# Kernel optimization log

Measured on AMD Instinct MI355X. Metric: run time of the kernel, lower is better.

The kernel has to match this reference:

```python
import jax, jax.numpy as jnp
import numpy as np

B, T, C = 16, 4096, 2048
H = 16
HS = C // H  # 128
SCALE = 1.0 / float(np.sqrt(HS))


def setup_inputs() -> dict:
    key = jax.random.key(0)
    k1, k2, k3, k4, k5 = jax.random.split(key, 5)
    x = jax.random.normal(k1, (B, 1, C), dtype=jnp.float32)
    k = jax.random.normal(k2, (B, H, T, HS), dtype=jnp.float32)
    v = jax.random.normal(k3, (B, H, T, HS), dtype=jnp.float32)
    # nn.Linear(dim, dim, bias=False) weights, applied as x @ W.T
    Wq = jax.random.normal(k4, (C, C), dtype=jnp.float32) * (1.0 / np.sqrt(C))
    Wp = jax.random.normal(k5, (C, C), dtype=jnp.float32) * (1.0 / np.sqrt(C))
    return {"x": x, "k": k, "v": v, "Wq": Wq, "Wp": Wp}


def reference(x, k, v, Wq, Wp):
    # decode branch: only last token of x is used
    q = x[:, -1, :] @ Wq.T                      # [B, C]
    q = q.reshape(B, H, HS)                     # [B, H, HS] (single query token)
    # att = (q * k).sum(-1) * scale  -> scores over cache length T
    att = jnp.einsum('bhd,bhtd->bht', q, k) * SCALE   # [B, H, T]
    att = jax.nn.softmax(att, axis=-1)
    # y = att @ v  -> [B, H, 1, HS], collapsed here
    y = jnp.einsum('bht,bhtd->bhd', att, v)     # [B, H, HS]
    y = y.reshape(B, 1, C)                      # transpose(1,2).view(B,1,C) equivalent for 1 token
    out = y @ Wp.T                              # [B, 1, C]; dropout is identity in eval
    return out
```

## Files before the change

### kernel.cpp

```cpp
#include <hip/hip_runtime.h>
#include <cmath>

#define C_DIM 2048
#define B_DIM 16
#define H_DIM 16
#define HS_DIM 128
#define T_DIM 4096
#define ATT_SCALE 0.08838834764831845f

__global__ __launch_bounds__(256) void gemv16_kernel(
    const float* __restrict__ X, const float* __restrict__ W,
    float* __restrict__ O) {
  const int lane = threadIdx.x & 63;
  const int wave = threadIdx.x >> 6;
  const int n = blockIdx.x * 4 + wave;
  const float* wrow = W + (size_t)n * C_DIM;

  float acc[B_DIM];
#pragma unroll
  for (int m = 0; m < B_DIM; ++m) acc[m] = 0.f;

#pragma unroll
  for (int i = 0; i < C_DIM / 256; ++i) {
    const int j = i * 256 + lane * 4;
    const float4 w4 = *reinterpret_cast<const float4*>(wrow + j);
#pragma unroll
    for (int m = 0; m < B_DIM; ++m) {
      const float4 x4 = *reinterpret_cast<const float4*>(X + m * C_DIM + j);
      acc[m] += w4.x * x4.x + w4.y * x4.y + w4.z * x4.z + w4.w * x4.w;
    }
  }

#pragma unroll
  for (int m = 0; m < B_DIM; ++m) {
#pragma unroll
    for (int mask = 32; mask >= 1; mask >>= 1)
      acc[m] += __shfl_xor(acc[m], mask, 64);
  }
  if (lane == 0) {
#pragma unroll
    for (int m = 0; m < B_DIM; ++m) O[(size_t)m * C_DIM + n] = acc[m];
  }
}

__global__ __launch_bounds__(1024) void attn_decode_kernel(
    const float* __restrict__ q, const float* __restrict__ k,
    const float* __restrict__ v, float* __restrict__ y) {
  const int bh = blockIdx.x;
  const int lane = threadIdx.x & 63;
  const int wave = threadIdx.x >> 6;
  const int half = lane >> 5;
  const int dl = lane & 31;

  const float4* kp = reinterpret_cast<const float4*>(k + (size_t)bh * T_DIM * HS_DIM);
  const float4* vp = reinterpret_cast<const float4*>(v + (size_t)bh * T_DIM * HS_DIM);
  const float4 qv = reinterpret_cast<const float4*>(q + (size_t)bh * HS_DIM)[dl];

  float m = -INFINITY, l = 0.f;
  float y0 = 0.f, y1 = 0.f, y2 = 0.f, y3 = 0.f;
  const int t0 = wave * (T_DIM / 16);

#pragma unroll 8
  for (int ti = 0; ti < T_DIM / 32; ++ti) {
    const int t = t0 + 2 * ti + half;
    const float4 kv = kp[(size_t)t * 32 + dl];
    const float4 vv = vp[(size_t)t * 32 + dl];
    float p = kv.x * qv.x + kv.y * qv.y + kv.z * qv.z + kv.w * qv.w;
#pragma unroll
    for (int mask = 16; mask >= 1; mask >>= 1) p += __shfl_xor(p, mask, 64);
    const float s = p * ATT_SCALE;
    const float mn = fmaxf(m, s);
    const float c = __expf(m - mn);
    const float e = __expf(s - mn);
    l = l * c + e;
    y0 = fmaf(y0, c, e * vv.x);
    y1 = fmaf(y1, c, e * vv.y);
    y2 = fmaf(y2, c, e * vv.z);
    y3 = fmaf(y3, c, e * vv.w);
    m = mn;
  }

  __shared__ float lm[32];
  __shared__ float ll[32];
  __shared__ float ly[32 * HS_DIM];
  float4* ly4 = reinterpret_cast<float4*>(ly);
  const int p32 = wave * 2 + half;
  ly4[p32 * 32 + dl] = make_float4(y0, y1, y2, y3);
  if (dl == 0) { lm[p32] = m; ll[p32] = l; }
  __syncthreads();

  if (wave == 0) {
    float gm = -INFINITY;
#pragma unroll
    for (int w = 0; w < 32; ++w) gm = fmaxf(gm, lm[w]);
    float L = 0.f, a0 = 0.f, a1 = 0.f;
#pragma unroll
    for (int w = 0; w < 32; ++w) {
      const float sc = __expf(lm[w] - gm);
      L += ll[w] * sc;
      a0 = fmaf(ly[w * HS_DIM + lane], sc, a0);
      a1 = fmaf(ly[w * HS_DIM + 64 + lane], sc, a1);
    }
    y[(size_t)bh * HS_DIM + lane] = a0 / L;
    y[(size_t)bh * HS_DIM + 64 + lane] = a1 / L;
  }
}

extern "C" void kernel_launch(void* const* d_in, const int* in_sizes, int n_in,
                              void* d_out, int out_size, void* d_ws, size_t ws_size,
                              hipStream_t stream) {
  const float* x  = (const float*)d_in[0];
  const float* k  = (const float*)d_in[1];
  const float* v  = (const float*)d_in[2];
  const float* Wq = (const float*)d_in[3];
  const float* Wp = (const float*)d_in[4];
  float* out = (float*)d_out;

  float* ws   = (float*)d_ws;
  float* q_ws = ws;
  float* y_ws = ws + B_DIM * C_DIM;

  hipLaunchKernelGGL(gemv16_kernel, dim3(C_DIM / 4), dim3(256), 0, stream,
                     x, Wq, q_ws);
  hipLaunchKernelGGL(attn_decode_kernel, dim3(B_DIM * H_DIM), dim3(1024), 0, stream,
                     q_ws, k, v, y_ws);
  hipLaunchKernelGGL(gemv16_kernel, dim3(C_DIM / 4), dim3(256), 0, stream,
                     y_ws, Wp, out);
}
```

Baseline: 278.0 us.

## Split attention decode over T chunks with separate combine kernel

```diff
diff --git a/kernel.cpp b/kernel.cpp
--- a/kernel.cpp
+++ b/kernel.cpp
@@ -7,6 +7,8 @@
 #define HS_DIM 128
 #define T_DIM 4096
 #define ATT_SCALE 0.08838834764831845f
+#define TCHUNK 512
+#define NCHUNK (T_DIM / TCHUNK)
 
 __global__ __launch_bounds__(256) void gemv16_kernel(
     const float* __restrict__ X, const float* __restrict__ W,
@@ -43,14 +45,18 @@
   }
 }
 
-__global__ __launch_bounds__(1024) void attn_decode_kernel(
+__global__ __launch_bounds__(256, 6) void attn_partial_kernel(
     const float* __restrict__ q, const float* __restrict__ k,
-    const float* __restrict__ v, float* __restrict__ y) {
-  const int bh = blockIdx.x;
+    const float* __restrict__ v, float* __restrict__ pm,
+    float* __restrict__ pl, float* __restrict__ py) {
+  const int blk = blockIdx.x;
+  const int bh = blk >> 3;
+  const int chunk = blk & 7;
   const int lane = threadIdx.x & 63;
   const int wave = threadIdx.x >> 6;
   const int half = lane >> 5;
   const int dl = lane & 31;
+  const int unit = wave * 2 + half;
 
   const float4* kp = reinterpret_cast<const float4*>(k + (size_t)bh * T_DIM * HS_DIM);
   const float4* vp = reinterpret_cast<const float4*>(v + (size_t)bh * T_DIM * HS_DIM);
@@ -58,11 +64,11 @@
 
   float m = -INFINITY, l = 0.f;
   float y0 = 0.f, y1 = 0.f, y2 = 0.f, y3 = 0.f;
-  const int t0 = wave * (T_DIM / 16);
+  const int tbase = chunk * TCHUNK + unit;
 
-#pragma unroll 8
-  for (int ti = 0; ti < T_DIM / 32; ++ti) {
-    const int t = t0 + 2 * ti + half;
+#pragma unroll 4
+  for (int ti = 0; ti < TCHUNK / 8; ++ti) {
+    const int t = tbase + ti * 8;
     const float4 kv = kp[(size_t)t * 32 + dl];
     const float4 vv = vp[(size_t)t * 32 + dl];
     float p = kv.x * qv.x + kv.y * qv.y + kv.z * qv.z + kv.w * qv.w;
@@ -80,30 +86,46 @@
     m = mn;
   }
 
-  __shared__ float lm[32];
-  __shared__ float ll[32];
-  __shared__ float ly[32 * HS_DIM];
-  float4* ly4 = reinterpret_cast<float4*>(ly);
-  const int p32 = wave * 2 + half;
-  ly4[p32 * 32 + dl] = make_float4(y0, y1, y2, y3);
-  if (dl == 0) { lm[p32] = m; ll[p32] = l; }
+  __shared__ float lm[8];
+  __shared__ float ll[8];
+  __shared__ float ly[8 * HS_DIM];
+  reinterpret_cast<float4*>(ly)[unit * 32 + dl] = make_float4(y0, y1, y2, y3);
+  if (dl == 0) { lm[unit] = m; ll[unit] = l; }
   __syncthreads();
 
-  if (wave == 0) {
-    float gm = -INFINITY;
+  const int tid = threadIdx.x;
+  if (tid < HS_DIM) {
+    float gm = lm[0];
 #pragma unroll
-    for (int w = 0; w < 32; ++w) gm = fmaxf(gm, lm[w]);
-    float L = 0.f, a0 = 0.f, a1 = 0.f;
+    for (int u = 1; u < 8; ++u) gm = fmaxf(gm, lm[u]);
+    float L = 0.f, yd = 0.f;
 #pragma unroll
-    for (int w = 0; w < 32; ++w) {
-      const float sc = __expf(lm[w] - gm);
-      L += ll[w] * sc;
-      a0 = fmaf(ly[w * HS_DIM + lane], sc, a0);
-      a1 = fmaf(ly[w * HS_DIM + 64 + lane], sc, a1);
+    for (int u = 0; u < 8; ++u) {
+      const float e = __expf(lm[u] - gm);
+      L = fmaf(e, ll[u], L);
+      yd = fmaf(e, ly[u * HS_DIM + tid], yd);
     }
-    y[(size_t)bh * HS_DIM + lane] = a0 / L;
-    y[(size_t)bh * HS_DIM + 64 + lane] = a1 / L;
+    py[(size_t)blk * HS_DIM + tid] = yd;
+    if (tid == 0) { pm[blk] = gm; pl[blk] = L; }
   }
+}
+
+__global__ __launch_bounds__(128) void attn_combine_kernel(
+    const float* __restrict__ pm, const float* __restrict__ pl,
+    const float* __restrict__ py, float* __restrict__ y) {
+  const int bh = blockIdx.x;
+  const int d = threadIdx.x;
+  float gm = -INFINITY;
+#pragma unroll
+  for (int c = 0; c < NCHUNK; ++c) gm = fmaxf(gm, pm[bh * NCHUNK + c]);
+  float L = 0.f, yd = 0.f;
+#pragma unroll
+  for (int c = 0; c < NCHUNK; ++c) {
+    const float e = __expf(pm[bh * NCHUNK + c] - gm);
+    L = fmaf(e, pl[bh * NCHUNK + c], L);
+    yd = fmaf(e, py[(size_t)(bh * NCHUNK + c) * HS_DIM + d], yd);
+  }
+  y[(size_t)bh * HS_DIM + d] = yd / L;
 }
 
 extern "C" void kernel_launch(void* const* d_in, const int* in_sizes, int n_in,
@@ -119,11 +141,16 @@
   float* ws   = (float*)d_ws;
   float* q_ws = ws;
   float* y_ws = ws + B_DIM * C_DIM;
+  float* pm   = y_ws + B_DIM * C_DIM;
+  float* pl   = pm + B_DIM * H_DIM * NCHUNK;
+  float* py   = pl + B_DIM * H_DIM * NCHUNK;
 
   hipLaunchKernelGGL(gemv16_kernel, dim3(C_DIM / 4), dim3(256), 0, stream,
                      x, Wq, q_ws);
-  hipLaunchKernelGGL(attn_decode_kernel, dim3(B_DIM * H_DIM), dim3(1024), 0, stream,
-                     q_ws, k, v, y_ws);
+  hipLaunchKernelGGL(attn_partial_kernel, dim3(B_DIM * H_DIM * NCHUNK), dim3(256), 0, stream,
+                     q_ws, k, v, pm, pl, py);
+  hipLaunchKernelGGL(attn_combine_kernel, dim3(B_DIM * H_DIM), dim3(128), 0, stream,
+                     pm, pl, py, y_ws);
   hipLaunchKernelGGL(gemv16_kernel, dim3(C_DIM / 4), dim3(256), 0, stream,
                      y_ws, Wp, out);
 }
```

Result: no change. 280.3 us (+0.8%).
